# Optimization experiments

Hardware: AMD Instinct MI355X
Metric: run time of the kernel (lower is better)

## Reference

```python
import jax, jax.numpy as jnp
import numpy as np

N, IN, HID, HEADS, HC, E, K = 50000, 512, 256, 8, 32, 600000, 4
EPS = 1e-5


def _gcn(h_in, W, b, src, dst):
    # PyG GCNConv: add self-loops, symmetric normalization, linear + bias
    h = h_in @ W  # [N, out]
    loop = jnp.arange(N)
    s = jnp.concatenate([src, loop])
    d = jnp.concatenate([dst, loop])
    deg = jax.ops.segment_sum(jnp.ones(s.shape[0], h.dtype), d, num_segments=N)
    dinv = jnp.where(deg > 0, jax.lax.rsqrt(deg), 0.0)
    msg = h[s] * (dinv[s] * dinv[d])[:, None]
    return jax.ops.segment_sum(msg, d, num_segments=N) + b


def _gat(h_in, W, a_src, a_dst, b, src, dst):
    # PyG GATConv: self-loops, LeakyReLU(0.2) logits, per-dst softmax, concat heads
    loop = jnp.arange(N)
    s = jnp.concatenate([src, loop])
    d = jnp.concatenate([dst, loop])
    h = (h_in @ W).reshape(N, HEADS, HC)
    e = jax.nn.leaky_relu((h * a_src).sum(-1)[s] + (h * a_dst).sum(-1)[d], 0.2)  # [E', H]
    m = jax.ops.segment_max(e, d, num_segments=N)  # every node has a self-loop
    ex = jnp.exp(e - m[d])
    alpha = ex / jax.ops.segment_sum(ex, d, num_segments=N)[d]
    out = jax.ops.segment_sum(h[s] * alpha[:, :, None], d, num_segments=N)  # [N, H, C]
    return out.reshape(N, HID) + b


def _ln(h, g, bta):
    mu = h.mean(-1, keepdims=True)
    var = ((h - mu) ** 2).mean(-1, keepdims=True)
    return (h - mu) * jax.lax.rsqrt(var + EPS) * g + bta


def _forward(x, style, stress, params, edges):
    (gW0, gb0, gW1, gb1, gW2, gb2, aW, aas, aad, ab, lg, lb, fW1, fb1, fW2, fb2) = params
    outs = []
    for k in range(K):
        src, dst = edges[k][0], edges[k][1]
        h = jax.nn.relu(_gcn(x, gW0[k], gb0[k], src, dst))
        h = jax.nn.relu(_gcn(h, gW1[k], gb1[k], src, dst))
        h = jax.nn.relu(_gcn(h, gW2[k], gb2[k], src, dst))
        h = _gat(h, aW[k], aas[k], aad[k], ab[k], src, dst)
        outs.append(_ln(h, lg[k], lb[k]))
    ctx = jnp.concatenate([style, stress], axis=-1)
    w = jax.nn.softmax(jnp.tanh(ctx @ fW1 + fb1) @ fW2 + fb2, axis=-1)  # [N, K]
    stacked = jnp.stack(outs, axis=1)  # [N, K, HID]
    return jnp.einsum('nk,nkd->nd', w, stacked)


def setup_inputs() -> dict:
    key = jax.random.key(0)
    ks = jax.random.split(key, 16)
    rn = lambda k, shape, s=0.05: jax.random.normal(k, shape, jnp.float32) * s
    return {
        "x": rn(ks[0], (N, IN), 1.0),
        "style_features": rn(ks[1], (N, HID), 1.0),
        "stress_features": rn(ks[2], (N, HID), 1.0),
        "edge_index0": jax.random.randint(ks[3], (2, E), 0, N),
        "edge_index1": jax.random.randint(ks[4], (2, E), 0, N),
        "edge_index2": jax.random.randint(ks[5], (2, E), 0, N),
        "edge_index3": jax.random.randint(ks[6], (2, E), 0, N),
        "gcn_W0": rn(ks[7], (K, IN, HID)),
        "gcn_b0": jnp.zeros((K, HID), jnp.float32),
        "gcn_W1": rn(ks[8], (K, HID, HID)),
        "gcn_b1": jnp.zeros((K, HID), jnp.float32),
        "gcn_W2": rn(ks[9], (K, HID, HID)),
        "gcn_b2": jnp.zeros((K, HID), jnp.float32),
        "gat_W": rn(ks[10], (K, HID, HID)),
        "gat_a_src": rn(ks[11], (K, HEADS, HC), 0.1),
        "gat_a_dst": rn(ks[12], (K, HEADS, HC), 0.1),
        "gat_b": jnp.zeros((K, HID), jnp.float32),
        "ln_g": jnp.ones((K, HID), jnp.float32),
        "ln_b": jnp.zeros((K, HID), jnp.float32),
        "fus_W1": rn(ks[13], (2 * HID, HID)),
        "fus_b1": jnp.zeros((HID,), jnp.float32),
        "fus_W2": rn(ks[14], (HID, K)),
        "fus_b2": jnp.zeros((K,), jnp.float32),
    }


def reference(x, edge_index0, edge_index1, edge_index2, edge_index3, style_features, stress_features, gcn_W0, gcn_b0, gcn_W1, gcn_b1, gcn_W2, gcn_b2, gat_W, gat_a_src, gat_a_dst, gat_b, ln_g, ln_b, fus_W1, fus_b1, fus_W2, fus_b2):
    params = (gcn_W0, gcn_b0, gcn_W1, gcn_b1, gcn_W2, gcn_b2, gat_W, gat_a_src, gat_a_dst, gat_b, ln_g, ln_b, fus_W1, fus_b1, fus_W2, fus_b2)
    edges = (edge_index0, edge_index1, edge_index2, edge_index3)
    return _forward(x, style_features, stress_features, params, edges)
```

## Files before the change

### kernel.cpp

```cpp
#include <hip/hip_runtime.h>
#include <hip/hip_bf16.h>
#include <cstdint>

#define N_NODES 50000
#define IN_DIM  512
#define HID     256
#define NEDGE   600000
#define TOPO    4
#define DEGMAX  96

typedef __attribute__((ext_vector_type(4))) float floatx4;
typedef _Float16 half4 __attribute__((ext_vector_type(4)));
typedef _Float16 half8 __attribute__((ext_vector_type(8)));

static __device__ __forceinline__ unsigned f2ord(float f) {
  unsigned b = __float_as_uint(f);
  return (b & 0x80000000u) ? ~b : (b | 0x80000000u);
}
static __device__ __forceinline__ float ord2f(unsigned u) {
  unsigned b = (u & 0x80000000u) ? (u & 0x7fffffffu) : ~u;
  return __uint_as_float(b);
}

__global__ void conv_f2h_kernel(const float* __restrict__ src, _Float16* __restrict__ dst, int n4) {
  int i = blockIdx.x * 256 + threadIdx.x;
  if (i < n4) {
    float4 v = ((const float4*)src)[i];
    half4 h;
    h[0] = (_Float16)v.x; h[1] = (_Float16)v.y; h[2] = (_Float16)v.z; h[3] = (_Float16)v.w;
    ((half4*)dst)[i] = h;
  }
}

__global__ void conv_ctx_kernel(const float* __restrict__ style, const float* __restrict__ stress,
                                _Float16* __restrict__ dst) {
  int i = blockIdx.x * 256 + threadIdx.x;
  if (i >= N_NODES * 128) return;
  int n = i >> 7, c4 = i & 127;
  int c = c4 * 4;
  const float* s = (c < 256) ? (style + (size_t)n * 256 + c) : (stress + (size_t)n * 256 + (c - 256));
  float4 v = *(const float4*)s;
  half4 h;
  h[0] = (_Float16)v.x; h[1] = (_Float16)v.y; h[2] = (_Float16)v.z; h[3] = (_Float16)v.w;
  ((half4*)(dst + (size_t)n * 512))[c4] = h;
}

#define WT_FUS 0
#define WT_G0  131072
#define WT_G1  655360
#define WT_G2  917504
#define WT_AW  1179648
#define WT_TOT 1441792
__global__ void wconv_all_kernel(const float* __restrict__ fW1, const float* __restrict__ gW0,
                                 const float* __restrict__ gW1, const float* __restrict__ gW2,
                                 const float* __restrict__ aW, _Float16* __restrict__ wt) {
  int idx = blockIdx.x * 256 + threadIdx.x;
  if (idx >= WT_TOT) return;
  const float* src;
  int local, sh;
  if (idx < WT_G0) { src = fW1; sh = 9; local = idx; }
  else if (idx < WT_G1) { int r = idx - WT_G0; src = gW0 + (size_t)(r >> 17) * 131072; sh = 9; local = r & 131071; }
  else if (idx < WT_G2) { int r = idx - WT_G1; src = gW1 + (size_t)(r >> 16) * 65536; sh = 8; local = r & 65535; }
  else if (idx < WT_AW) { int r = idx - WT_G2; src = gW2 + (size_t)(r >> 16) * 65536; sh = 8; local = r & 65535; }
  else { int r = idx - WT_AW; src = aW + (size_t)(r >> 16) * 65536; sh = 8; local = r & 65535; }
  int n = local >> sh;
  int kd = local & ((1 << sh) - 1);
  wt[idx] = (_Float16)src[(size_t)kd * 256 + n];
}

template <int KD>
__global__ __launch_bounds__(256, 3) void gemm_f16_kernel(
    const _Float16* __restrict__ A, const _Float16* __restrict__ Wt,
    const float* __restrict__ bias, _Float16* __restrict__ C, int M, int mode,
    const float* __restrict__ scale) {
  constexpr int NIT = KD / 32;
  __shared__ __align__(16) _Float16 As[2][2048];
  const int tid = threadIdx.x;
  const int lane = tid & 63;
  const int wv = tid >> 6;
  const int mr = lane & 15;
  const int q = (lane >> 4) & 3;
  const int r0 = blockIdx.x * 64;

  int arow = r0 + ((tid >> 6) * 16) + (tid & 15);
  if (arow > M - 1) arow = M - 1;
  const _Float16* pa = A + (size_t)arow * KD + ((tid >> 4) & 3) * 8;
  const _Float16* pb[4];
#pragma unroll
  for (int t = 0; t < 4; ++t)
    pb[t] = Wt + (size_t)((wv * 4 + t) * 16 + mr) * KD + q * 8;

  floatx4 acc[4][4];
#pragma unroll
  for (int g = 0; g < 4; ++g)
#pragma unroll
    for (int t = 0; t < 4; ++t) acc[g][t] = (floatx4){0.f, 0.f, 0.f, 0.f};

  half8 a0, a1, b0[4], b1[4];
  a0 = *(const half8*)pa; pa += 32;
#pragma unroll
  for (int t = 0; t < 4; ++t) { b0[t] = *(const half8*)pb[t]; pb[t] += 32; }
  *(half8*)&As[0][(unsigned)tid * 8] = a0;
  if (NIT > 1) { a1 = *(const half8*)pa; pa += 32; }
  __syncthreads();

#pragma unroll 1
  for (int it = 0; it < NIT; it += 2) {
    if (it + 1 < NIT) {
      *(half8*)&As[1][(unsigned)tid * 8] = a1;
#pragma unroll
      for (int t = 0; t < 4; ++t) { b1[t] = *(const half8*)pb[t]; pb[t] += 32; }
      if (it + 2 < NIT) { a0 = *(const half8*)pa; pa += 32; }
    }
    {
      half8 af[4];
#pragma unroll
      for (int g = 0; g < 4; ++g) af[g] = *(const half8*)&As[0][(g * 64 + lane) * 8];
#pragma unroll
      for (int g = 0; g < 4; ++g)
#pragma unroll
        for (int t = 0; t < 4; ++t)
          acc[g][t] = __builtin_amdgcn_mfma_f32_16x16x32_f16(b0[t], af[g], acc[g][t], 0, 0, 0);
    }
    if (it + 1 < NIT) {
      __syncthreads();
      if (it + 2 < NIT) {
        *(half8*)&As[0][(unsigned)tid * 8] = a0;
#pragma unroll
        for (int t = 0; t < 4; ++t) { b0[t] = *(const half8*)pb[t]; pb[t] += 32; }
        if (it + 3 < NIT) { a1 = *(const half8*)pa; pa += 32; }
      }
      half8 af[4];
#pragma unroll
      for (int g = 0; g < 4; ++g) af[g] = *(const half8*)&As[1][(g * 64 + lane) * 8];
#pragma unroll
      for (int g = 0; g < 4; ++g)
#pragma unroll
        for (int t = 0; t < 4; ++t)
          acc[g][t] = __builtin_amdgcn_mfma_f32_16x16x32_f16(b1[t], af[g], acc[g][t], 0, 0, 0);
      if (it + 2 < NIT) __syncthreads();
    }
  }

  float sv[4];
#pragma unroll
  for (int g = 0; g < 4; ++g) {
    int row = r0 + g * 16 + mr;
    sv[g] = (scale && row < M) ? scale[row] : 1.f;
  }
#pragma unroll
  for (int t = 0; t < 4; ++t) {
    int c0 = (wv * 4 + t) * 16 + q * 4;
    float4 bv;
    if (bias) bv = *(const float4*)&bias[c0];
    else { bv.x = 0.f; bv.y = 0.f; bv.z = 0.f; bv.w = 0.f; }
#pragma unroll
    for (int g = 0; g < 4; ++g) {
      int row = r0 + g * 16 + mr;
      if (row < M) {
        half4 o;
#pragma unroll
        for (int r = 0; r < 4; ++r) {
          float v = acc[g][t][r] + (&bv.x)[r];
          if (mode == 1) v = tanhf(v);
          v *= sv[g];
          o[r] = (_Float16)v;
        }
        *(half4*)&C[(size_t)row * HID + c0] = o;
      }
    }
  }
}

__global__ void zero_int_kernel(int* p, int n, unsigned* gmax) {
  int i = blockIdx.x * 256 + threadIdx.x;
  if (i < n) p[i] = 0;
  if (blockIdx.x == 0 && threadIdx.x < 8) gmax[threadIdx.x] = 0u;
}
__global__ void fill_kernel(const int* __restrict__ src, const int* __restrict__ dst,
                            int* __restrict__ cur, int* __restrict__ csr_src, int n) {
  int i = blockIdx.x * 256 + threadIdx.x;
  if (i < n) {
    int d = dst[i];
    int slot = atomicAdd(&cur[d], 1);
    if (slot < DEGMAX) csr_src[(size_t)d * DEGMAX + slot] = src[i];
  }
}
__global__ void dinv_kernel(const int* __restrict__ deg, float* __restrict__ dinv, int n) {
  int i = blockIdx.x * 256 + threadIdx.x;
  if (i < n) dinv[i] = rsqrtf((float)(deg[i] + 1));
}

__global__ __launch_bounds__(256) void gcn_agg_kernel(
    const _Float16* __restrict__ hlin, const int* __restrict__ deg,
    const int* __restrict__ csr_src, const float* __restrict__ dinv,
    const float* __restrict__ bias, _Float16* __restrict__ out) {
  int w = (int)((blockIdx.x * blockDim.x + threadIdx.x) >> 6);
  int lane = threadIdx.x & 63;
  if (w >= N_NODES) return;
  float dv = dinv[w];
  half4 hv = ((const half4*)(hlin + (size_t)w * HID))[lane];
  float A0 = (float)hv[0], A1 = (float)hv[1], A2 = (float)hv[2], A3 = (float)hv[3];
  float B0 = 0.f, B1 = 0.f, B2 = 0.f, B3 = 0.f;
  float C0 = 0.f, C1 = 0.f, C2 = 0.f, C3 = 0.f;
  float D0 = 0.f, D1 = 0.f, D2 = 0.f, D3 = 0.f;
  int dg = deg[w];
  if (dg > DEGMAX) dg = DEGMAX;
  const int* sp = csr_src + (size_t)w * DEGMAX;
  int s = 0;
  for (; s + 4 <= dg; s += 4) {
    int4 iv = *(const int4*)(sp + s);
    half4 v0 = ((const half4*)(hlin + (size_t)iv.x * HID))[lane];
    half4 v1 = ((const half4*)(hlin + (size_t)iv.y * HID))[lane];
    half4 v2 = ((const half4*)(hlin + (size_t)iv.z * HID))[lane];
    half4 v3 = ((const half4*)(hlin + (size_t)iv.w * HID))[lane];
    A0 += (float)v0[0]; A1 += (float)v0[1]; A2 += (float)v0[2]; A3 += (float)v0[3];
    B0 += (float)v1[0]; B1 += (float)v1[1]; B2 += (float)v1[2]; B3 += (float)v1[3];
    C0 += (float)v2[0]; C1 += (float)v2[1]; C2 += (float)v2[2]; C3 += (float)v2[3];
    D0 += (float)v3[0]; D1 += (float)v3[1]; D2 += (float)v3[2]; D3 += (float)v3[3];
  }
  for (; s < dg; ++s) {
    half4 v = ((const half4*)(hlin + (size_t)sp[s] * HID))[lane];
    A0 += (float)v[0]; A1 += (float)v[1]; A2 += (float)v[2]; A3 += (float)v[3];
  }
  float4 b = ((const float4*)bias)[lane];
  half4 r;
  r[0] = (_Float16)fmaxf((A0 + B0 + C0 + D0) * dv + b.x, 0.f);
  r[1] = (_Float16)fmaxf((A1 + B1 + C1 + D1) * dv + b.y, 0.f);
  r[2] = (_Float16)fmaxf((A2 + B2 + C2 + D2) * dv + b.z, 0.f);
  r[3] = (_Float16)fmaxf((A3 + B3 + C3 + D3) * dv + b.w, 0.f);
  ((half4*)(out + (size_t)w * HID))[lane] = r;
}

__global__ __launch_bounds__(256) void gat_prep_kernel(
    const _Float16* __restrict__ hlin, const float* __restrict__ a_src,
    const float* __restrict__ a_dst, float* __restrict__ asad) {
  int w = (int)((blockIdx.x * blockDim.x + threadIdx.x) >> 6);
  int lane = threadIdx.x & 63;
  if (w >= N_NODES) return;
  half4 h = ((const half4*)(hlin + (size_t)w * HID))[lane];
  float4 s4 = ((const float4*)a_src)[lane];
  float4 d4 = ((const float4*)a_dst)[lane];
  float hx = h[0], hy = h[1], hz = h[2], hw = h[3];
  float ps = hx * s4.x + hy * s4.y + hz * s4.z + hw * s4.w;
  float pd = hx * d4.x + hy * d4.y + hz * d4.z + hw * d4.w;
  for (int o = 1; o < 8; o <<= 1) { ps += __shfl_xor(ps, o, 64); pd += __shfl_xor(pd, o, 64); }
  if ((lane & 7) == 0) {
    int hh = lane >> 3;
    asad[(size_t)w * 16 + hh] = ps;
    asad[(size_t)w * 16 + 8 + hh] = pd;
  }
}

__global__ __launch_bounds__(256) void gmax_kernel(const float* __restrict__ asad,
                                                   unsigned* __restrict__ gmax) {
  int t = threadIdx.x;
  int h = t & 7;
  float m = -1e30f;
  for (int n = blockIdx.x * 32 + (t >> 3); n < N_NODES; n += gridDim.x * 32)
    m = fmaxf(m, asad[(size_t)n * 16 + h]);
  m = fmaxf(m, __shfl_xor(m, 8, 64));
  m = fmaxf(m, __shfl_xor(m, 16, 64));
  m = fmaxf(m, __shfl_xor(m, 32, 64));
  if ((t & 63) < 8) atomicMax(&gmax[h], f2ord(m));
}

static __device__ __forceinline__ float lrelu(float e) {
  return e > 0.f ? e : 0.2f * e;
}

__global__ __launch_bounds__(256) void gat_agg_kernel(
    const _Float16* __restrict__ hlin, const int* __restrict__ deg,
    const int* __restrict__ csr_src, const float* __restrict__ asad,
    const unsigned* __restrict__ gmax, const float* __restrict__ bias,
    const float* __restrict__ lng, const float* __restrict__ lnb,
    const float* __restrict__ wsel, int kk, float* __restrict__ dout) {
  int w = (int)((blockIdx.x * blockDim.x + threadIdx.x) >> 6);
  int lane = threadIdx.x & 63;
  if (w >= N_NODES) return;
  int head = lane >> 3;
  float ad_d = asad[(size_t)w * 16 + 8 + head];
  float m = lrelu(ord2f(gmax[head]) + ad_d);
  float e_self = lrelu(asad[(size_t)w * 16 + head] + ad_d);
  int dg = deg[w];
  if (dg > DEGMAX) dg = DEGMAX;
  const int* sp = csr_src + (size_t)w * DEGMAX;
  float lA = __expf(e_self - m), lB = 0.f, lC = 0.f, lD = 0.f;
  half4 hv = ((const half4*)(hlin + (size_t)w * HID))[lane];
  float A0 = (float)hv[0] * lA, A1 = (float)hv[1] * lA,
        A2 = (float)hv[2] * lA, A3 = (float)hv[3] * lA;
  float B0 = 0.f, B1 = 0.f, B2 = 0.f, B3 = 0.f;
  float C0 = 0.f, C1 = 0.f, C2 = 0.f, C3 = 0.f;
  float D0 = 0.f, D1 = 0.f, D2 = 0.f, D3 = 0.f;
  int s = 0;
  for (; s + 4 <= dg; s += 4) {
    int4 iv = *(const int4*)(sp + s);
    float w0 = __expf(lrelu(asad[(size_t)iv.x * 16 + head] + ad_d) - m);
    float w1 = __expf(lrelu(asad[(size_t)iv.y * 16 + head] + ad_d) - m);
    float w2 = __expf(lrelu(asad[(size_t)iv.z * 16 + head] + ad_d) - m);
    float w3 = __expf(lrelu(asad[(size_t)iv.w * 16 + head] + ad_d) - m);
    half4 v0 = ((const half4*)(hlin + (size_t)iv.x * HID))[lane];
    half4 v1 = ((const half4*)(hlin + (size_t)iv.y * HID))[lane];
    half4 v2 = ((const half4*)(hlin + (size_t)iv.z * HID))[lane];
    half4 v3 = ((const half4*)(hlin + (size_t)iv.w * HID))[lane];
    lA += w0; lB += w1; lC += w2; lD += w3;
    A0 += (float)v0[0] * w0; A1 += (float)v0[1] * w0; A2 += (float)v0[2] * w0; A3 += (float)v0[3] * w0;
    B0 += (float)v1[0] * w1; B1 += (float)v1[1] * w1; B2 += (float)v1[2] * w1; B3 += (float)v1[3] * w1;
    C0 += (float)v2[0] * w2; C1 += (float)v2[1] * w2; C2 += (float)v2[2] * w2; C3 += (float)v2[3] * w2;
    D0 += (float)v3[0] * w3; D1 += (float)v3[1] * w3; D2 += (float)v3[2] * w3; D3 += (float)v3[3] * w3;
  }
  for (; s < dg; ++s) {
    int sc = sp[s];
    float w0 = __expf(lrelu(asad[(size_t)sc * 16 + head] + ad_d) - m);
    half4 v = ((const half4*)(hlin + (size_t)sc * HID))[lane];
    lA += w0;
    A0 += (float)v[0] * w0; A1 += (float)v[1] * w0;
    A2 += (float)v[2] * w0; A3 += (float)v[3] * w0;
  }
  float inv = 1.f / (lA + lB + lC + lD);
  float4 b = ((const float4*)bias)[lane];
  float vx = (A0 + B0 + C0 + D0) * inv + b.x;
  float vy = (A1 + B1 + C1 + D1) * inv + b.y;
  float vz = (A2 + B2 + C2 + D2) * inv + b.z;
  float vw = (A3 + B3 + C3 + D3) * inv + b.w;
  float ssum = vx + vy + vz + vw;
  for (int o = 1; o < 64; o <<= 1) ssum += __shfl_xor(ssum, o, 64);
  float mu = ssum * (1.f / HID);
  float dx = vx - mu, dy = vy - mu, dz = vz - mu, dw = vw - mu;
  float qq = dx * dx + dy * dy + dz * dz + dw * dw;
  for (int o = 1; o < 64; o <<= 1) qq += __shfl_xor(qq, o, 64);
  float rs = rsqrtf(qq * (1.f / HID) + 1e-5f);
  float4 g4 = ((const float4*)lng)[lane];
  float4 b4 = ((const float4*)lnb)[lane];
  float wk = wsel[(size_t)w * 4 + kk];
  float4 r;
  r.x = (dx * rs * g4.x + b4.x) * wk;
  r.y = (dy * rs * g4.y + b4.y) * wk;
  r.z = (dz * rs * g4.z + b4.z) * wk;
  r.w = (dw * rs * g4.w + b4.w) * wk;
  float4* dp = (float4*)(dout + (size_t)w * HID) + lane;
  if (kk == 0) {
    *dp = r;
  } else {
    float4 old = *dp;
    old.x += r.x; old.y += r.y; old.z += r.z; old.w += r.w;
    *dp = old;
  }
}

__global__ __launch_bounds__(256) void fusw_kernel(
    const _Float16* __restrict__ t, const float* __restrict__ W2,
    const float* __restrict__ b2, float* __restrict__ wout) {
  int w = (int)((blockIdx.x * blockDim.x + threadIdx.x) >> 6);
  int lane = threadIdx.x & 63;
  if (w >= N_NODES) return;
  half4 t4h = ((const half4*)(t + (size_t)w * HID))[lane];
  float tx = t4h[0], ty = t4h[1], tz = t4h[2], tw = t4h[3];
  int c = lane * 4;
  float4 w0 = ((const float4*)W2)[c + 0];
  float4 w1 = ((const float4*)W2)[c + 1];
  float4 w2 = ((const float4*)W2)[c + 2];
  float4 w3 = ((const float4*)W2)[c + 3];
  float p0 = tx * w0.x + ty * w1.x + tz * w2.x + tw * w3.x;
  float p1 = tx * w0.y + ty * w1.y + tz * w2.y + tw * w3.y;
  float p2 = tx * w0.z + ty * w1.z + tz * w2.z + tw * w3.z;
  float p3 = tx * w0.w + ty * w1.w + tz * w2.w + tw * w3.w;
  for (int o = 1; o < 64; o <<= 1) {
    p0 += __shfl_xor(p0, o, 64); p1 += __shfl_xor(p1, o, 64);
    p2 += __shfl_xor(p2, o, 64); p3 += __shfl_xor(p3, o, 64);
  }
  if (lane == 0) {
    p0 += b2[0]; p1 += b2[1]; p2 += b2[2]; p3 += b2[3];
    float mx = fmaxf(fmaxf(p0, p1), fmaxf(p2, p3));
    float e0 = __expf(p0 - mx), e1 = __expf(p1 - mx), e2 = __expf(p2 - mx), e3 = __expf(p3 - mx);
    float inv = 1.f / (e0 + e1 + e2 + e3);
    float4 r; r.x = e0 * inv; r.y = e1 * inv; r.z = e2 * inv; r.w = e3 * inv;
    ((float4*)wout)[w] = r;
  }
}

extern "C" void kernel_launch(void* const* d_in, const int* in_sizes, int n_in,
                              void* d_out, int out_size, void* d_ws, size_t ws_size,
                              hipStream_t stream) {
  const float* x      = (const float*)d_in[0];
  const float* style  = (const float*)d_in[1];
  const float* stress = (const float*)d_in[2];
  const int* edges[4] = {(const int*)d_in[3], (const int*)d_in[4],
                         (const int*)d_in[5], (const int*)d_in[6]};
  const float* gW0 = (const float*)d_in[7];
  const float* gb0 = (const float*)d_in[8];
  const float* gW1 = (const float*)d_in[9];
  const float* gb1 = (const float*)d_in[10];
  const float* gW2 = (const float*)d_in[11];
  const float* gb2 = (const float*)d_in[12];
  const float* aW  = (const float*)d_in[13];
  const float* aas = (const float*)d_in[14];
  const float* aad = (const float*)d_in[15];
  const float* ab  = (const float*)d_in[16];
  const float* lg  = (const float*)d_in[17];
  const float* lb  = (const float*)d_in[18];
  const float* fW1 = (const float*)d_in[19];
  const float* fb1 = (const float*)d_in[20];
  const float* fW2 = (const float*)d_in[21];
  const float* fb2 = (const float*)d_in[22];
  float* out = (float*)d_out;
  (void)in_sizes; (void)n_in; (void)out_size; (void)ws_size;

  char* wsp = (char*)d_ws;
  size_t off = 0;
  auto alloc = [&](size_t bytes) -> void* {
    void* p = wsp + off;
    off += (bytes + 255) & ~(size_t)255;
    return p;
  };
  _Float16* h_act = (_Float16*)alloc((size_t)N_NODES * HID * 2);
  _Float16* h_lin = (_Float16*)alloc((size_t)N_NODES * HID * 2);
  _Float16* x_h   = (_Float16*)alloc((size_t)N_NODES * IN_DIM * 2);
  _Float16* wtall = (_Float16*)alloc((size_t)WT_TOT * 2);
  float* wsel = (float*)alloc((size_t)N_NODES * 4 * 4);
  float* dinv = (float*)alloc((size_t)N_NODES * 4);
  int* cur = (int*)alloc((size_t)N_NODES * 4);
  float* asad = (float*)alloc((size_t)N_NODES * 16 * 4);
  unsigned* gmax = (unsigned*)alloc(256);
  char* shared_region = (char*)alloc((size_t)N_NODES * IN_DIM * 2);
  _Float16* ctx_h = (_Float16*)shared_region;
  int* csr_src = (int*)shared_region;

  dim3 blk(256);
  const int nodeWaveBlocks = N_NODES / 4;
  const int nBlocksN = (N_NODES + 255) / 256;
  const int nBlocksE = (NEDGE + 255) / 256;
  const int gemmBlocks = (N_NODES + 63) / 64;

  conv_f2h_kernel<<<(N_NODES * IN_DIM / 4 + 255) / 256, blk, 0, stream>>>(x, x_h, N_NODES * IN_DIM / 4);
  conv_ctx_kernel<<<(N_NODES * 128 + 255) / 256, blk, 0, stream>>>(style, stress, ctx_h);
  wconv_all_kernel<<<(WT_TOT + 255) / 256, blk, 0, stream>>>(fW1, gW0, gW1, gW2, aW, wtall);

  gemm_f16_kernel<512><<<gemmBlocks, blk, 0, stream>>>(ctx_h, wtall + WT_FUS, fb1, h_lin, N_NODES, 1, nullptr);
  fusw_kernel<<<nodeWaveBlocks, blk, 0, stream>>>(h_lin, fW2, fb2, wsel);

  for (int k = 0; k < TOPO; ++k) {
    const int* srcp = edges[k];
    const int* dstp = edges[k] + NEDGE;
    zero_int_kernel<<<nBlocksN, blk, 0, stream>>>(cur, N_NODES, gmax);
    fill_kernel<<<nBlocksE, blk, 0, stream>>>(srcp, dstp, cur, csr_src, NEDGE);
    dinv_kernel<<<nBlocksN, blk, 0, stream>>>(cur, dinv, N_NODES);

    gemm_f16_kernel<512><<<gemmBlocks, blk, 0, stream>>>(
        x_h, wtall + WT_G0 + (size_t)k * 131072, nullptr, h_lin, N_NODES, 0, dinv);
    gcn_agg_kernel<<<nodeWaveBlocks, blk, 0, stream>>>(h_lin, cur, csr_src, dinv,
                                                       gb0 + (size_t)k * HID, h_act);
    gemm_f16_kernel<256><<<gemmBlocks, blk, 0, stream>>>(
        h_act, wtall + WT_G1 + (size_t)k * 65536, nullptr, h_lin, N_NODES, 0, dinv);
    gcn_agg_kernel<<<nodeWaveBlocks, blk, 0, stream>>>(h_lin, cur, csr_src, dinv,
                                                       gb1 + (size_t)k * HID, h_act);
    gemm_f16_kernel<256><<<gemmBlocks, blk, 0, stream>>>(
        h_act, wtall + WT_G2 + (size_t)k * 65536, nullptr, h_lin, N_NODES, 0, dinv);
    gcn_agg_kernel<<<nodeWaveBlocks, blk, 0, stream>>>(h_lin, cur, csr_src, dinv,
                                                       gb2 + (size_t)k * HID, h_act);
    gemm_f16_kernel<256><<<gemmBlocks, blk, 0, stream>>>(
        h_act, wtall + WT_AW + (size_t)k * 65536, nullptr, h_lin, N_NODES, 0, nullptr);
    gat_prep_kernel<<<nodeWaveBlocks, blk, 0, stream>>>(h_lin, aas + (size_t)k * HID,
                                                        aad + (size_t)k * HID, asad);
    gmax_kernel<<<64, blk, 0, stream>>>(asad, gmax);
    gat_agg_kernel<<<nodeWaveBlocks, blk, 0, stream>>>(h_lin, cur, csr_src, asad, gmax,
                                                       ab + (size_t)k * HID,
                                                       lg + (size_t)k * HID,
                                                       lb + (size_t)k * HID,
                                                       wsel, k, out);
  }
}
```

Before: 1.950 ms.

## Batch first-layer GEMMs across topologies, prefetch gathers, share GAT edge weights

When the workspace is large enough, the first-layer x@W0 GEMM for all four topologies is launched once as a 2D grid before the loop. Because that GEMM no longer knows each topology's dinv, the GCN aggregation applies source-side dinv per neighbour. Separately, the GCN aggregation loop now software-pipelines its neighbour gathers one group ahead. The GAT aggregation computes each edge's attention exp once per (edge, head) lane and broadcasts it with shuffles, replacing the redundant per-lane exp and separate tail loop. This trades a larger workspace and extra dinv gathers for fewer launches, better GEMM occupancy and less repeated exp work.

```diff
diff --git a/kernel.cpp b/kernel.cpp
--- a/kernel.cpp
+++ b/kernel.cpp
@@ -70,10 +70,12 @@
 
 template <int KD>
 __global__ __launch_bounds__(256, 3) void gemm_f16_kernel(
-    const _Float16* __restrict__ A, const _Float16* __restrict__ Wt,
-    const float* __restrict__ bias, _Float16* __restrict__ C, int M, int mode,
-    const float* __restrict__ scale) {
+    const _Float16* __restrict__ A, const _Float16* __restrict__ Wt0,
+    const float* __restrict__ bias, _Float16* __restrict__ C0, int M, int mode,
+    const float* __restrict__ scale, int wt_stride, int c_stride) {
   constexpr int NIT = KD / 32;
+  const _Float16* Wt = Wt0 + (size_t)blockIdx.y * wt_stride;
+  _Float16* C = C0 + (size_t)blockIdx.y * c_stride;
   __shared__ __align__(16) _Float16 As[2][2048];
   const int tid = threadIdx.x;
   const int lane = tid & 63;
@@ -191,6 +193,7 @@
   if (i < n) dinv[i] = rsqrtf((float)(deg[i] + 1));
 }
 
+template <int PRESCALED>
 __global__ __launch_bounds__(256) void gcn_agg_kernel(
     const _Float16* __restrict__ hlin, const int* __restrict__ deg,
     const int* __restrict__ csr_src, const float* __restrict__ dinv,
@@ -200,7 +203,9 @@
   if (w >= N_NODES) return;
   float dv = dinv[w];
   half4 hv = ((const half4*)(hlin + (size_t)w * HID))[lane];
-  float A0 = (float)hv[0], A1 = (float)hv[1], A2 = (float)hv[2], A3 = (float)hv[3];
+  float selfs = PRESCALED ? 1.f : dv;
+  float A0 = (float)hv[0] * selfs, A1 = (float)hv[1] * selfs,
+        A2 = (float)hv[2] * selfs, A3 = (float)hv[3] * selfs;
   float B0 = 0.f, B1 = 0.f, B2 = 0.f, B3 = 0.f;
   float C0 = 0.f, C1 = 0.f, C2 = 0.f, C3 = 0.f;
   float D0 = 0.f, D1 = 0.f, D2 = 0.f, D3 = 0.f;
@@ -208,20 +213,54 @@
   if (dg > DEGMAX) dg = DEGMAX;
   const int* sp = csr_src + (size_t)w * DEGMAX;
   int s = 0;
-  for (; s + 4 <= dg; s += 4) {
-    int4 iv = *(const int4*)(sp + s);
-    half4 v0 = ((const half4*)(hlin + (size_t)iv.x * HID))[lane];
-    half4 v1 = ((const half4*)(hlin + (size_t)iv.y * HID))[lane];
-    half4 v2 = ((const half4*)(hlin + (size_t)iv.z * HID))[lane];
-    half4 v3 = ((const half4*)(hlin + (size_t)iv.w * HID))[lane];
-    A0 += (float)v0[0]; A1 += (float)v0[1]; A2 += (float)v0[2]; A3 += (float)v0[3];
-    B0 += (float)v1[0]; B1 += (float)v1[1]; B2 += (float)v1[2]; B3 += (float)v1[3];
-    C0 += (float)v2[0]; C1 += (float)v2[1]; C2 += (float)v2[2]; C3 += (float)v2[3];
-    D0 += (float)v3[0]; D1 += (float)v3[1]; D2 += (float)v3[2]; D3 += (float)v3[3];
+  if (dg >= 4) {
+    int4 iv = *(const int4*)sp;
+    half4 p0 = ((const half4*)(hlin + (size_t)iv.x * HID))[lane];
+    half4 p1 = ((const half4*)(hlin + (size_t)iv.y * HID))[lane];
+    half4 p2 = ((const half4*)(hlin + (size_t)iv.z * HID))[lane];
+    half4 p3 = ((const half4*)(hlin + (size_t)iv.w * HID))[lane];
+    float e0 = 1.f, e1 = 1.f, e2 = 1.f, e3 = 1.f;
+    if (!PRESCALED) { e0 = dinv[iv.x]; e1 = dinv[iv.y]; e2 = dinv[iv.z]; e3 = dinv[iv.w]; }
+    for (s = 4; s + 4 <= dg; s += 4) {
+      int4 nx = *(const int4*)(sp + s);
+      half4 q0 = ((const half4*)(hlin + (size_t)nx.x * HID))[lane];
+      half4 q1 = ((const half4*)(hlin + (size_t)nx.y * HID))[lane];
+      half4 q2 = ((const half4*)(hlin + (size_t)nx.z * HID))[lane];
+      half4 q3 = ((const half4*)(hlin + (size_t)nx.w * HID))[lane];
+      float f0 = 1.f, f1 = 1.f, f2 = 1.f, f3 = 1.f;
+      if (!PRESCALED) { f0 = dinv[nx.x]; f1 = dinv[nx.y]; f2 = dinv[nx.z]; f3 = dinv[nx.w]; }
+      if (PRESCALED) {
+        A0 += (float)p0[0]; A1 += (float)p0[1]; A2 += (float)p0[2]; A3 += (float)p0[3];
+        B0 += (float)p1[0]; B1 += (float)p1[1]; B2 += (float)p1[2]; B3 += (float)p1[3];
+        C0 += (float)p2[0]; C1 += (float)p2[1]; C2 += (float)p2[2]; C3 += (float)p2[3];
+        D0 += (float)p3[0]; D1 += (float)p3[1]; D2 += (float)p3[2]; D3 += (float)p3[3];
+      } else {
+        A0 += (float)p0[0] * e0; A1 += (float)p0[1] * e0; A2 += (float)p0[2] * e0; A3 += (float)p0[3] * e0;
+        B0 += (float)p1[0] * e1; B1 += (float)p1[1] * e1; B2 += (float)p1[2] * e1; B3 += (float)p1[3] * e1;
+        C0 += (float)p2[0] * e2; C1 += (float)p2[1] * e2; C2 += (float)p2[2] * e2; C3 += (float)p2[3] * e2;
+        D0 += (float)p3[0] * e3; D1 += (float)p3[1] * e3; D2 += (float)p3[2] * e3; D3 += (float)p3[3] * e3;
+      }
+      p0 = q0; p1 = q1; p2 = q2; p3 = q3;
+      e0 = f0; e1 = f1; e2 = f2; e3 = f3;
+    }
+    if (PRESCALED) {
+      A0 += (float)p0[0]; A1 += (float)p0[1]; A2 += (float)p0[2]; A3 += (float)p0[3];
+      B0 += (float)p1[0]; B1 += (float)p1[1]; B2 += (float)p1[2]; B3 += (float)p1[3];
+      C0 += (float)p2[0]; C1 += (float)p2[1]; C2 += (float)p2[2]; C3 += (float)p2[3];
+      D0 += (float)p3[0]; D1 += (float)p3[1]; D2 += (float)p3[2]; D3 += (float)p3[3];
+    } else {
+      A0 += (float)p0[0] * e0; A1 += (float)p0[1] * e0; A2 += (float)p0[2] * e0; A3 += (float)p0[3] * e0;
+      B0 += (float)p1[0] * e1; B1 += (float)p1[1] * e1; B2 += (float)p1[2] * e1; B3 += (float)p1[3] * e1;
+      C0 += (float)p2[0] * e2; C1 += (float)p2[1] * e2; C2 += (float)p2[2] * e2; C3 += (float)p2[3] * e2;
+      D0 += (float)p3[0] * e3; D1 += (float)p3[1] * e3; D2 += (float)p3[2] * e3; D3 += (float)p3[3] * e3;
+    }
   }
   for (; s < dg; ++s) {
-    half4 v = ((const half4*)(hlin + (size_t)sp[s] * HID))[lane];
-    A0 += (float)v[0]; A1 += (float)v[1]; A2 += (float)v[2]; A3 += (float)v[3];
+    int sc = sp[s];
+    float nr = PRESCALED ? 1.f : dinv[sc];
+    half4 v = ((const half4*)(hlin + (size_t)sc * HID))[lane];
+    A0 += (float)v[0] * nr; A1 += (float)v[1] * nr;
+    A2 += (float)v[2] * nr; A3 += (float)v[3] * nr;
   }
   float4 b = ((const float4*)bias)[lane];
   half4 r;
@@ -279,9 +318,13 @@
   int lane = threadIdx.x & 63;
   if (w >= N_NODES) return;
   int head = lane >> 3;
+  int e7 = lane & 7;
+  int gsel = lane >> 4;
   float ad_d = asad[(size_t)w * 16 + 8 + head];
   float m = lrelu(ord2f(gmax[head]) + ad_d);
   float e_self = lrelu(asad[(size_t)w * 16 + head] + ad_d);
+  float ad_e = __shfl(ad_d, e7 << 3, 64);
+  float m_e = __shfl(m, e7 << 3, 64);
   int dg = deg[w];
   if (dg > DEGMAX) dg = DEGMAX;
   const int* sp = csr_src + (size_t)w * DEGMAX;
@@ -292,30 +335,42 @@
   float B0 = 0.f, B1 = 0.f, B2 = 0.f, B3 = 0.f;
   float C0 = 0.f, C1 = 0.f, C2 = 0.f, C3 = 0.f;
   float D0 = 0.f, D1 = 0.f, D2 = 0.f, D3 = 0.f;
-  int s = 0;
-  for (; s + 4 <= dg; s += 4) {
-    int4 iv = *(const int4*)(sp + s);
-    float w0 = __expf(lrelu(asad[(size_t)iv.x * 16 + head] + ad_d) - m);
-    float w1 = __expf(lrelu(asad[(size_t)iv.y * 16 + head] + ad_d) - m);
-    float w2 = __expf(lrelu(asad[(size_t)iv.z * 16 + head] + ad_d) - m);
-    float w3 = __expf(lrelu(asad[(size_t)iv.w * 16 + head] + ad_d) - m);
+  int ng = (dg + 3) >> 2;
+  int4 iv;
+  if (ng) iv = *(const int4*)sp;
+  for (int gi = 0; gi < ng; ++gi) {
+    int s4 = gi << 2;
+    int rem = dg - s4;
+    bool tail = rem < 4;
+    if (tail) {
+      if (rem < 2) iv.y = iv.x;
+      if (rem < 3) iv.z = iv.x;
+      iv.w = iv.x;
+    }
+    int nsel = gsel == 0 ? iv.x : gsel == 1 ? iv.y : gsel == 2 ? iv.z : iv.w;
+    float av = asad[(size_t)nsel * 16 + e7];
     half4 v0 = ((const half4*)(hlin + (size_t)iv.x * HID))[lane];
     half4 v1 = ((const half4*)(hlin + (size_t)iv.y * HID))[lane];
     half4 v2 = ((const half4*)(hlin + (size_t)iv.z * HID))[lane];
     half4 v3 = ((const half4*)(hlin + (size_t)iv.w * HID))[lane];
+    int4 nx = iv;
+    if (gi + 1 < ng) nx = *(const int4*)(sp + s4 + 4);
+    float ve = __expf(lrelu(av + ad_e) - m_e);
+    float w0 = __shfl(ve, head, 64);
+    float w1 = __shfl(ve, 16 + head, 64);
+    float w2 = __shfl(ve, 32 + head, 64);
+    float w3 = __shfl(ve, 48 + head, 64);
+    if (tail) {
+      if (rem < 2) w1 = 0.f;
+      if (rem < 3) w2 = 0.f;
+      w3 = 0.f;
+    }
     lA += w0; lB += w1; lC += w2; lD += w3;
     A0 += (float)v0[0] * w0; A1 += (float)v0[1] * w0; A2 += (float)v0[2] * w0; A3 += (float)v0[3] * w0;
     B0 += (float)v1[0] * w1; B1 += (float)v1[1] * w1; B2 += (float)v1[2] * w1; B3 += (float)v1[3] * w1;
     C0 += (float)v2[0] * w2; C1 += (float)v2[1] * w2; C2 += (float)v2[2] * w2; C3 += (float)v2[3] * w2;
     D0 += (float)v3[0] * w3; D1 += (float)v3[1] * w3; D2 += (float)v3[2] * w3; D3 += (float)v3[3] * w3;
-  }
-  for (; s < dg; ++s) {
-    int sc = sp[s];
-    float w0 = __expf(lrelu(asad[(size_t)sc * 16 + head] + ad_d) - m);
-    half4 v = ((const half4*)(hlin + (size_t)sc * HID))[lane];
-    lA += w0;
-    A0 += (float)v[0] * w0; A1 += (float)v[1] * w0;
-    A2 += (float)v[2] * w0; A3 += (float)v[3] * w0;
+    iv = nx;
   }
   float inv = 1.f / (lA + lB + lC + lD);
   float4 b = ((const float4*)bias)[lane];
@@ -404,7 +459,7 @@
   const float* fW2 = (const float*)d_in[21];
   const float* fb2 = (const float*)d_in[22];
   float* out = (float*)d_out;
-  (void)in_sizes; (void)n_in; (void)out_size; (void)ws_size;
+  (void)in_sizes; (void)n_in; (void)out_size;
 
   char* wsp = (char*)d_ws;
   size_t off = 0;
@@ -413,18 +468,41 @@
     off += (bytes + 255) & ~(size_t)255;
     return p;
   };
-  _Float16* h_act = (_Float16*)alloc((size_t)N_NODES * HID * 2);
-  _Float16* h_lin = (_Float16*)alloc((size_t)N_NODES * HID * 2);
-  _Float16* x_h   = (_Float16*)alloc((size_t)N_NODES * IN_DIM * 2);
+  auto al = [](size_t b) { return (b + 255) & ~(size_t)255; };
+
+  const size_t sz_hact = (size_t)N_NODES * HID * 2;
+  const size_t sz_xh   = (size_t)N_NODES * IN_DIM * 2;
+  const size_t sz_csr  = (size_t)N_NODES * DEGMAX * 4;
+  const size_t sz_hlin0 = (size_t)4 * N_NODES * HID * 2;
+
+  const size_t fixed = al(sz_hact) * 2 + al(sz_xh) + al((size_t)WT_TOT * 2) +
+                       al((size_t)N_NODES * 16) + al((size_t)N_NODES * 4) * 2 +
+                       al((size_t)N_NODES * 64) + al(256);
+  const size_t need_hoist = fixed + al(sz_csr) + al(sz_hlin0);
+  const bool hoist = ws_size >= need_hoist;
+
+  _Float16* h_act = (_Float16*)alloc(sz_hact);
+  _Float16* h_lin = (_Float16*)alloc(sz_hact);
+  _Float16* x_h   = (_Float16*)alloc(sz_xh);
   _Float16* wtall = (_Float16*)alloc((size_t)WT_TOT * 2);
-  float* wsel = (float*)alloc((size_t)N_NODES * 4 * 4);
+  float* wsel = (float*)alloc((size_t)N_NODES * 16);
   float* dinv = (float*)alloc((size_t)N_NODES * 4);
   int* cur = (int*)alloc((size_t)N_NODES * 4);
-  float* asad = (float*)alloc((size_t)N_NODES * 16 * 4);
+  float* asad = (float*)alloc((size_t)N_NODES * 64);
   unsigned* gmax = (unsigned*)alloc(256);
-  char* shared_region = (char*)alloc((size_t)N_NODES * IN_DIM * 2);
-  _Float16* ctx_h = (_Float16*)shared_region;
-  int* csr_src = (int*)shared_region;
+  _Float16* ctx_h;
+  int* csr_src;
+  _Float16* h_lin0 = nullptr;
+  if (hoist) {
+    csr_src = (int*)alloc(sz_csr);
+    char* region = (char*)alloc(sz_hlin0);
+    ctx_h = (_Float16*)region;
+    h_lin0 = (_Float16*)region;
+  } else {
+    char* shared_region = (char*)alloc(sz_xh);
+    ctx_h = (_Float16*)shared_region;
+    csr_src = (int*)shared_region;
+  }
 
   dim3 blk(256);
   const int nodeWaveBlocks = N_NODES / 4;
@@ -436,8 +514,15 @@
   conv_ctx_kernel<<<(N_NODES * 128 + 255) / 256, blk, 0, stream>>>(style, stress, ctx_h);
   wconv_all_kernel<<<(WT_TOT + 255) / 256, blk, 0, stream>>>(fW1, gW0, gW1, gW2, aW, wtall);
 
-  gemm_f16_kernel<512><<<gemmBlocks, blk, 0, stream>>>(ctx_h, wtall + WT_FUS, fb1, h_lin, N_NODES, 1, nullptr);
+  gemm_f16_kernel<512><<<gemmBlocks, blk, 0, stream>>>(ctx_h, wtall + WT_FUS, fb1, h_lin,
+                                                       N_NODES, 1, nullptr, 0, 0);
   fusw_kernel<<<nodeWaveBlocks, blk, 0, stream>>>(h_lin, fW2, fb2, wsel);
+
+  if (hoist) {
+    gemm_f16_kernel<512><<<dim3(gemmBlocks, 4), blk, 0, stream>>>(
+        x_h, wtall + WT_G0, nullptr, h_lin0, N_NODES, 0, nullptr,
+        131072, N_NODES * HID);
+  }
 
   for (int k = 0; k < TOPO; ++k) {
     const int* srcp = edges[k];
@@ -446,20 +531,26 @@
     fill_kernel<<<nBlocksE, blk, 0, stream>>>(srcp, dstp, cur, csr_src, NEDGE);
     dinv_kernel<<<nBlocksN, blk, 0, stream>>>(cur, dinv, N_NODES);
 
-    gemm_f16_kernel<512><<<gemmBlocks, blk, 0, stream>>>(
-        x_h, wtall + WT_G0 + (size_t)k * 131072, nullptr, h_lin, N_NODES, 0, dinv);
-    gcn_agg_kernel<<<nodeWaveBlocks, blk, 0, stream>>>(h_lin, cur, csr_src, dinv,
-                                                       gb0 + (size_t)k * HID, h_act);
+    if (hoist) {
+      gcn_agg_kernel<0><<<nodeWaveBlocks, blk, 0, stream>>>(
+          h_lin0 + (size_t)k * N_NODES * HID, cur, csr_src, dinv,
+          gb0 + (size_t)k * HID, h_act);
+    } else {
+      gemm_f16_kernel<512><<<gemmBlocks, blk, 0, stream>>>(
+          x_h, wtall + WT_G0 + (size_t)k * 131072, nullptr, h_lin, N_NODES, 0, dinv, 0, 0);
+      gcn_agg_kernel<1><<<nodeWaveBlocks, blk, 0, stream>>>(h_lin, cur, csr_src, dinv,
+                                                            gb0 + (size_t)k * HID, h_act);
+    }
     gemm_f16_kernel<256><<<gemmBlocks, blk, 0, stream>>>(
-        h_act, wtall + WT_G1 + (size_t)k * 65536, nullptr, h_lin, N_NODES, 0, dinv);
-    gcn_agg_kernel<<<nodeWaveBlocks, blk, 0, stream>>>(h_lin, cur, csr_src, dinv,
-                                                       gb1 + (size_t)k * HID, h_act);
+        h_act, wtall + WT_G1 + (size_t)k * 65536, nullptr, h_lin, N_NODES, 0, dinv, 0, 0);
+    gcn_agg_kernel<1><<<nodeWaveBlocks, blk, 0, stream>>>(h_lin, cur, csr_src, dinv,
+                                                          gb1 + (size_t)k * HID, h_act);
     gemm_f16_kernel<256><<<gemmBlocks, blk, 0, stream>>>(
-        h_act, wtall + WT_G2 + (size_t)k * 65536, nullptr, h_lin, N_NODES, 0, dinv);
-    gcn_agg_kernel<<<nodeWaveBlocks, blk, 0, stream>>>(h_lin, cur, csr_src, dinv,
-                                                       gb2 + (size_t)k * HID, h_act);
+        h_act, wtall + WT_G2 + (size_t)k * 65536, nullptr, h_lin, N_NODES, 0, dinv, 0, 0);
+    gcn_agg_kernel<1><<<nodeWaveBlocks, blk, 0, stream>>>(h_lin, cur, csr_src, dinv,
+                                                          gb2 + (size_t)k * HID, h_act);
     gemm_f16_kernel<256><<<gemmBlocks, blk, 0, stream>>>(
-        h_act, wtall + WT_AW + (size_t)k * 65536, nullptr, h_lin, N_NODES, 0, nullptr);
+        h_act, wtall + WT_AW + (size_t)k * 65536, nullptr, h_lin, N_NODES, 0, nullptr, 0, 0);
     gat_prep_kernel<<<nodeWaveBlocks, blk, 0, stream>>>(h_lin, aas + (size_t)k * HID,
                                                         aad + (size_t)k * HID, asad);
     gmax_kernel<<<64, blk, 0, stream>>>(asad, gmax);
```

Result: faster. 1.902 ms (-2.4%).
